# Performance work log

Hardware: AMD Instinct MI355X
Metric: run time of the kernel (lower is better)

The kernel has to match this reference:

```python
import jax, jax.numpy as jnp
import numpy as np

B, T, C, H = 32, 2048, 1024, 64


def setup_inputs() -> dict:
    key = jax.random.key(0)
    k1, k2, k3, k4 = jax.random.split(key, 4)
    x = jax.random.normal(k1, (B, T, C), dtype=jnp.float32)
    # nn.Linear(C, H, bias=False) weights, stored here as [C, H] for x @ W
    s = 1.0 / np.sqrt(C)
    Wk = jax.random.uniform(k2, (C, H), jnp.float32, -s, s)
    Wq = jax.random.uniform(k3, (C, H), jnp.float32, -s, s)
    Wv = jax.random.uniform(k4, (C, H), jnp.float32, -s, s)
    return {"x": x, "Wk": Wk, "Wq": Wq, "Wv": Wv}


def reference(x, Wk, Wq, Wv):
    # projections: [B,T,C] @ [C,H] -> [B,T,H]
    k = jnp.einsum('btc,ch->bth', x, Wk)
    q = jnp.einsum('btc,ch->bth', x, Wq)
    v = jnp.einsum('btc,ch->bth', x, Wv)
    Hd = k.shape[-1]
    # attention scores [B,T,T], scaled by head_size^-0.5
    scores = jnp.einsum('bqh,bkh->bqk', q, k) * (Hd ** -0.5)
    # causal mask: masked_fill where triu(ones, 1)==1 -> -inf (mask strict upper triangle)
    Tq = x.shape[1]
    causal = jnp.tril(jnp.ones((Tq, Tq), dtype=bool))  # True = keep
    scores = jnp.where(causal, scores, -jnp.inf)
    attn = jax.nn.softmax(scores, axis=-1)
    # dropout: identity in eval/reference mode
    out = jnp.einsum('bqk,bkh->bqh', attn, v)
    return out
```

## Files before the change

kernel.cpp:

```cpp
#include <hip/hip_runtime.h>

typedef short bf16x8 __attribute__((ext_vector_type(8)));
typedef float f32x4 __attribute__((ext_vector_type(4)));

#define B_ 32
#define T_ 2048
#define C_ 1024
#define H_ 64

__device__ __forceinline__ ushort f2bf(float f) {
  union { float f; unsigned u; } v; v.f = f;
  unsigned u = v.u;
  return (ushort)((u + 0x7FFFu + ((u >> 16) & 1u)) >> 16);
}

__device__ __forceinline__ void async_copy16(void* lds, const void* g) {
  __builtin_amdgcn_global_load_lds(
      (const __attribute__((address_space(1))) unsigned int*)g,
      (__attribute__((address_space(3))) unsigned int*)lds, 16, 0, 0);
}

__global__ __launch_bounds__(256) void wconv_kernel(
    const float* __restrict__ Wk, const float* __restrict__ Wq,
    const float* __restrict__ Wv, ushort* __restrict__ Wt) {
  int idx = blockIdx.x * 256 + threadIdx.x;
  if (idx >= 3 * 64 * C_) return;
  int n = idx >> 10, c = idx & 1023;
  int mat = n >> 6, h = n & 63;
  const float* W = (mat == 0) ? Wk : (mat == 1 ? Wq : Wv);
  float v = W[c * 64 + h];
  if (mat == 1) v *= 0.18033688011112042f;
  Wt[idx] = f2bf(v);
}

__global__ __launch_bounds__(256) void qkv_kernel(
    const float* __restrict__ x, const ushort* __restrict__ Wt,
    ushort* __restrict__ Kb, ushort* __restrict__ Qb, ushort* __restrict__ Vt) {
  __shared__ __align__(16) float As[128 * 64];
  __shared__ __align__(16) ushort Bs[192 * 64];
  int tid = threadIdx.x;
  int wave = tid >> 6, lane = tid & 63, quad = lane >> 4, l16 = lane & 15;
  int r0 = blockIdx.x * 128;

  f32x4 acc[2][12];
#pragma unroll
  for (int rt = 0; rt < 2; ++rt)
#pragma unroll
    for (int nt = 0; nt < 12; ++nt) acc[rt][nt] = (f32x4){0.f, 0.f, 0.f, 0.f};

  for (int k0 = 0; k0 < C_; k0 += 64) {
    __syncthreads();
#pragma unroll
    for (int i = 0; i < 8; ++i) {
      int id = tid + 256 * i;
      int arow = id >> 4, acp = id & 15;
      int ac = acp ^ (arow & 15);
      async_copy16((char*)As + id * 16,
                   x + (size_t)(r0 + arow) * C_ + k0 + ac * 4);
    }
#pragma unroll
    for (int i = 0; i < 6; ++i) {
      int id = tid + 256 * i;
      int bn = id >> 3, bcp = id & 7;
      int bc = bcp ^ (bn & 7);
      async_copy16((char*)Bs + id * 16,
                   Wt + (size_t)bn * C_ + k0 + bc * 8);
    }
    __syncthreads();

#pragma unroll
    for (int ks = 0; ks < 2; ++ks) {
      bf16x8 af[2];
#pragma unroll
      for (int rt = 0; rt < 2; ++rt) {
        int row = wave * 32 + rt * 16 + l16;
        int c0 = ks * 8 + quad * 2;
        f32x4 a0 = *(const f32x4*)(As + row * 64 + ((c0 ^ l16) << 2));
        f32x4 a1 = *(const f32x4*)(As + row * 64 + (((c0 + 1) ^ l16) << 2));
        bf16x8 t;
        t[0] = (short)f2bf(a0[0]); t[1] = (short)f2bf(a0[1]);
        t[2] = (short)f2bf(a0[2]); t[3] = (short)f2bf(a0[3]);
        t[4] = (short)f2bf(a1[0]); t[5] = (short)f2bf(a1[1]);
        t[6] = (short)f2bf(a1[2]); t[7] = (short)f2bf(a1[3]);
        af[rt] = t;
      }
#pragma unroll
      for (int nt = 0; nt < 12; ++nt) {
        int n = nt * 16 + l16;
        int cb = ks * 4 + quad;
        bf16x8 bf = *(const bf16x8*)(Bs + n * 64 + ((cb ^ (l16 & 7)) << 3));
        acc[0][nt] = __builtin_amdgcn_mfma_f32_16x16x32_bf16(af[0], bf, acc[0][nt], 0, 0, 0);
        acc[1][nt] = __builtin_amdgcn_mfma_f32_16x16x32_bf16(af[1], bf, acc[1][nt], 0, 0, 0);
      }
    }
  }

  int b = r0 >> 11;
#pragma unroll
  for (int rt = 0; rt < 2; ++rt) {
    int rowbase = r0 + wave * 32 + rt * 16 + quad * 4;
#pragma unroll
    for (int nt = 0; nt < 12; ++nt) {
      int mat = nt >> 2;
      int h = (nt & 3) * 16 + l16;
#pragma unroll
      for (int r = 0; r < 4; ++r) {
        ushort val = f2bf(acc[rt][nt][r]);
        int row = rowbase + r;
        if (mat == 0)      Kb[(size_t)row * H_ + h] = val;
        else if (mat == 1) Qb[(size_t)row * H_ + h] = val;
        else               Vt[(size_t)b * H_ * T_ + (size_t)h * T_ + (row & (T_ - 1))] = val;
      }
    }
  }
}

__global__ __launch_bounds__(256) void attn_kernel(
    const ushort* __restrict__ Qb, const ushort* __restrict__ Kb,
    const ushort* __restrict__ Vt, float* __restrict__ out) {
  __shared__ __align__(16) ushort Pl[4 * 32 * 80];

  int tid = threadIdx.x;
  int wave = tid >> 6, lane = tid & 63, quad = lane >> 4, l16 = lane & 15;
  int batch = blockIdx.y;
  int q0 = blockIdx.x * 128 + wave * 32;
  const ushort* Qbase = Qb + (size_t)batch * T_ * H_;
  const ushort* Kbase = Kb + (size_t)batch * T_ * H_;
  const ushort* Vbase = Vt + (size_t)batch * H_ * T_;
  ushort* Pw = Pl + wave * 32 * 80;

  bf16x8 qf[2][2];
#pragma unroll
  for (int rt = 0; rt < 2; ++rt) {
    const ushort* qr = Qbase + (size_t)(q0 + rt * 16 + l16) * H_;
    qf[rt][0] = *(const bf16x8*)(qr + quad * 8);
    qf[rt][1] = *(const bf16x8*)(qr + 32 + quad * 8);
  }

  f32x4 o[2][4];
  float m_i[2][4], l_i[2][4];
#pragma unroll
  for (int rt = 0; rt < 2; ++rt)
#pragma unroll
    for (int i = 0; i < 4; ++i) {
      o[rt][i] = (f32x4){0.f, 0.f, 0.f, 0.f};
      m_i[rt][i] = -1e30f; l_i[rt][i] = 0.f;
    }

  int jb_last = (q0 + 31) >> 6;
  for (int jb = 0; jb <= jb_last; ++jb) {
    int j0 = jb * 64;

    f32x4 sv[2][4];
#pragma unroll
    for (int nt = 0; nt < 4; ++nt) {
      const ushort* kr = Kbase + (size_t)(j0 + nt * 16 + l16) * H_;
      bf16x8 kf0 = *(const bf16x8*)(kr + quad * 8);
      bf16x8 kf1 = *(const bf16x8*)(kr + 32 + quad * 8);
#pragma unroll
      for (int rt = 0; rt < 2; ++rt) {
        f32x4 z = (f32x4){0.f, 0.f, 0.f, 0.f};
        z = __builtin_amdgcn_mfma_f32_16x16x32_bf16(qf[rt][0], kf0, z, 0, 0, 0);
        z = __builtin_amdgcn_mfma_f32_16x16x32_bf16(qf[rt][1], kf1, z, 0, 0, 0);
        sv[rt][nt] = z;
      }
    }

    if (jb == jb_last) {
#pragma unroll
      for (int rt = 0; rt < 2; ++rt) {
        int rowg = q0 + rt * 16 + quad * 4;
#pragma unroll
        for (int nt = 0; nt < 4; ++nt) {
          int col = j0 + nt * 16 + l16;
#pragma unroll
          for (int rr = 0; rr < 4; ++rr)
            if (col > rowg + rr) sv[rt][nt][rr] = -1e30f;
        }
      }
    }

    float alpha[2][4];
#pragma unroll
    for (int rt = 0; rt < 2; ++rt)
#pragma unroll
      for (int rr = 0; rr < 4; ++rr) {
        float v = fmaxf(fmaxf(sv[rt][0][rr], sv[rt][1][rr]),
                        fmaxf(sv[rt][2][rr], sv[rt][3][rr]));
        v = fmaxf(v, __shfl_xor(v, 1));
        v = fmaxf(v, __shfl_xor(v, 2));
        v = fmaxf(v, __shfl_xor(v, 4));
        v = fmaxf(v, __shfl_xor(v, 8));
        float mn = fmaxf(m_i[rt][rr], v);
        alpha[rt][rr] = exp2f(m_i[rt][rr] - mn);
        m_i[rt][rr] = mn;
      }

#pragma unroll
    for (int rt = 0; rt < 2; ++rt) {
      float rsum[4] = {0.f, 0.f, 0.f, 0.f};
#pragma unroll
      for (int nt = 0; nt < 4; ++nt)
#pragma unroll
        for (int rr = 0; rr < 4; ++rr) {
          float p = exp2f(sv[rt][nt][rr] - m_i[rt][rr]);
          rsum[rr] += p;
          Pw[(rt * 16 + quad * 4 + rr) * 80 + nt * 16 + l16] = f2bf(p);
        }
#pragma unroll
      for (int rr = 0; rr < 4; ++rr)
        l_i[rt][rr] = alpha[rt][rr] * l_i[rt][rr] + rsum[rr];
#pragma unroll
      for (int ht = 0; ht < 4; ++ht)
#pragma unroll
        for (int rr = 0; rr < 4; ++rr) o[rt][ht][rr] *= alpha[rt][rr];
    }

    bf16x8 pf[2][2];
#pragma unroll
    for (int rt = 0; rt < 2; ++rt) {
      pf[rt][0] = *(const bf16x8*)(&Pw[(rt * 16 + l16) * 80 + quad * 8]);
      pf[rt][1] = *(const bf16x8*)(&Pw[(rt * 16 + l16) * 80 + 32 + quad * 8]);
    }
#pragma unroll
    for (int ht = 0; ht < 4; ++ht) {
      const ushort* vr = Vbase + (size_t)(ht * 16 + l16) * T_ + j0;
      bf16x8 vf0 = *(const bf16x8*)(vr + quad * 8);
      bf16x8 vf1 = *(const bf16x8*)(vr + 32 + quad * 8);
#pragma unroll
      for (int rt = 0; rt < 2; ++rt) {
        o[rt][ht] = __builtin_amdgcn_mfma_f32_16x16x32_bf16(pf[rt][0], vf0, o[rt][ht], 0, 0, 0);
        o[rt][ht] = __builtin_amdgcn_mfma_f32_16x16x32_bf16(pf[rt][1], vf1, o[rt][ht], 0, 0, 0);
      }
    }
  }

#pragma unroll
  for (int rt = 0; rt < 2; ++rt)
#pragma unroll
    for (int rr = 0; rr < 4; ++rr) {
      float v = l_i[rt][rr];
      v += __shfl_xor(v, 1);
      v += __shfl_xor(v, 2);
      v += __shfl_xor(v, 4);
      v += __shfl_xor(v, 8);
      l_i[rt][rr] = v;
    }
#pragma unroll
  for (int rt = 0; rt < 2; ++rt) {
    int rowbase = q0 + rt * 16 + quad * 4;
#pragma unroll
    for (int ht = 0; ht < 4; ++ht)
#pragma unroll
      for (int rr = 0; rr < 4; ++rr)
        out[((size_t)batch * T_ + rowbase + rr) * H_ + ht * 16 + l16] =
            o[rt][ht][rr] / l_i[rt][rr];
  }
}

extern "C" void kernel_launch(void* const* d_in, const int* in_sizes, int n_in,
                              void* d_out, int out_size, void* d_ws, size_t ws_size,
                              hipStream_t stream) {
  const float* x  = (const float*)d_in[0];
  const float* Wk = (const float*)d_in[1];
  const float* Wq = (const float*)d_in[2];
  const float* Wv = (const float*)d_in[3];
  float* out = (float*)d_out;

  ushort* Wt = (ushort*)d_ws;
  ushort* Kb = (ushort*)((char*)d_ws + (1 << 19));
  ushort* Qb = Kb + (size_t)B_ * T_ * H_;
  ushort* Vt = Qb + (size_t)B_ * T_ * H_;

  hipLaunchKernelGGL(wconv_kernel, dim3(768), dim3(256), 0, stream, Wk, Wq, Wv, Wt);
  hipLaunchKernelGGL(qkv_kernel, dim3(512), dim3(256), 0, stream, x, Wt, Kb, Qb, Vt);
  hipLaunchKernelGGL(attn_kernel, dim3(16, 32), dim3(256), 0, stream, Qb, Kb, Vt, out);
}
```

Measured before the change: 514.6 us.

## Restructure QKV projection staging and shrink attention tiles to one 16-row strip per wave

Result: slower. 667.3 us (+29.7%).

```diff
diff --git a/kernel.cpp b/kernel.cpp
--- a/kernel.cpp
+++ b/kernel.cpp
@@ -36,8 +36,7 @@
 __global__ __launch_bounds__(256) void qkv_kernel(
     const float* __restrict__ x, const ushort* __restrict__ Wt,
     ushort* __restrict__ Kb, ushort* __restrict__ Qb, ushort* __restrict__ Vt) {
-  __shared__ __align__(16) float As[128 * 64];
-  __shared__ __align__(16) ushort Bs[192 * 64];
+  __shared__ __align__(16) float As[2][128 * 64];
   int tid = threadIdx.x;
   int wave = tid >> 6, lane = tid & 63, quad = lane >> 4, l16 = lane & 15;
   int r0 = blockIdx.x * 128;
@@ -48,49 +47,52 @@
 #pragma unroll
     for (int nt = 0; nt < 12; ++nt) acc[rt][nt] = (f32x4){0.f, 0.f, 0.f, 0.f};
 
-  for (int k0 = 0; k0 < C_; k0 += 64) {
+  for (int k0 = 0; k0 < C_; k0 += 128) {
     __syncthreads();
 #pragma unroll
     for (int i = 0; i < 8; ++i) {
       int id = tid + 256 * i;
-      int arow = id >> 4, acp = id & 15;
-      int ac = acp ^ (arow & 15);
-      async_copy16((char*)As + id * 16,
-                   x + (size_t)(r0 + arow) * C_ + k0 + ac * 4);
-    }
-#pragma unroll
-    for (int i = 0; i < 6; ++i) {
+      int r = id >> 4, p = id & 15;
+      int c = p ^ (r & 15);
+      async_copy16((char*)(&As[0][0]) + id * 16,
+                   x + (size_t)(r0 + r) * C_ + k0 + c * 4);
+    }
+#pragma unroll
+    for (int i = 0; i < 8; ++i) {
       int id = tid + 256 * i;
-      int bn = id >> 3, bcp = id & 7;
-      int bc = bcp ^ (bn & 7);
-      async_copy16((char*)Bs + id * 16,
-                   Wt + (size_t)bn * C_ + k0 + bc * 8);
+      int r = id >> 4, p = id & 15;
+      int c = p ^ (r & 15);
+      async_copy16((char*)(&As[1][0]) + id * 16,
+                   x + (size_t)(r0 + r) * C_ + k0 + 64 + c * 4);
     }
     __syncthreads();
 
 #pragma unroll
-    for (int ks = 0; ks < 2; ++ks) {
-      bf16x8 af[2];
-#pragma unroll
-      for (int rt = 0; rt < 2; ++rt) {
-        int row = wave * 32 + rt * 16 + l16;
-        int c0 = ks * 8 + quad * 2;
-        f32x4 a0 = *(const f32x4*)(As + row * 64 + ((c0 ^ l16) << 2));
-        f32x4 a1 = *(const f32x4*)(As + row * 64 + (((c0 + 1) ^ l16) << 2));
-        bf16x8 t;
-        t[0] = (short)f2bf(a0[0]); t[1] = (short)f2bf(a0[1]);
-        t[2] = (short)f2bf(a0[2]); t[3] = (short)f2bf(a0[3]);
-        t[4] = (short)f2bf(a1[0]); t[5] = (short)f2bf(a1[1]);
-        t[6] = (short)f2bf(a1[2]); t[7] = (short)f2bf(a1[3]);
-        af[rt] = t;
-      }
-#pragma unroll
-      for (int nt = 0; nt < 12; ++nt) {
-        int n = nt * 16 + l16;
-        int cb = ks * 4 + quad;
-        bf16x8 bf = *(const bf16x8*)(Bs + n * 64 + ((cb ^ (l16 & 7)) << 3));
-        acc[0][nt] = __builtin_amdgcn_mfma_f32_16x16x32_bf16(af[0], bf, acc[0][nt], 0, 0, 0);
-        acc[1][nt] = __builtin_amdgcn_mfma_f32_16x16x32_bf16(af[1], bf, acc[1][nt], 0, 0, 0);
+    for (int half = 0; half < 2; ++half) {
+      int kbase = k0 + half * 64;
+#pragma unroll
+      for (int ks = 0; ks < 2; ++ks) {
+        bf16x8 af[2];
+#pragma unroll
+        for (int rt = 0; rt < 2; ++rt) {
+          int row = wave * 32 + rt * 16 + l16;
+          int c0 = ks * 8 + quad * 2;
+          f32x4 a0 = *(const f32x4*)(&As[half][row * 64 + ((c0 ^ l16) << 2)]);
+          f32x4 a1 = *(const f32x4*)(&As[half][row * 64 + (((c0 + 1) ^ l16) << 2)]);
+          bf16x8 t;
+          t[0] = (short)f2bf(a0[0]); t[1] = (short)f2bf(a0[1]);
+          t[2] = (short)f2bf(a0[2]); t[3] = (short)f2bf(a0[3]);
+          t[4] = (short)f2bf(a1[0]); t[5] = (short)f2bf(a1[1]);
+          t[6] = (short)f2bf(a1[2]); t[7] = (short)f2bf(a1[3]);
+          af[rt] = t;
+        }
+#pragma unroll
+        for (int nt = 0; nt < 12; ++nt) {
+          bf16x8 bf = *(const bf16x8*)(Wt + (size_t)(nt * 16 + l16) * C_ +
+                                       kbase + ks * 32 + quad * 8);
+          acc[0][nt] = __builtin_amdgcn_mfma_f32_16x16x32_bf16(af[0], bf, acc[0][nt], 0, 0, 0);
+          acc[1][nt] = __builtin_amdgcn_mfma_f32_16x16x32_bf16(af[1], bf, acc[1][nt], 0, 0, 0);
+        }
       }
     }
   }
@@ -103,13 +105,16 @@
     for (int nt = 0; nt < 12; ++nt) {
       int mat = nt >> 2;
       int h = (nt & 3) * 16 + l16;
-#pragma unroll
-      for (int r = 0; r < 4; ++r) {
-        ushort val = f2bf(acc[rt][nt][r]);
-        int row = rowbase + r;
-        if (mat == 0)      Kb[(size_t)row * H_ + h] = val;
-        else if (mat == 1) Qb[(size_t)row * H_ + h] = val;
-        else               Vt[(size_t)b * H_ * T_ + (size_t)h * T_ + (row & (T_ - 1))] = val;
+      if (mat == 2) {
+        ushort4 pv;
+        pv.x = f2bf(acc[rt][nt][0]); pv.y = f2bf(acc[rt][nt][1]);
+        pv.z = f2bf(acc[rt][nt][2]); pv.w = f2bf(acc[rt][nt][3]);
+        *(ushort4*)(&Vt[(size_t)b * H_ * T_ + (size_t)h * T_ + (rowbase & (T_ - 1))]) = pv;
+      } else {
+        ushort* dst = (mat == 0) ? Kb : Qb;
+#pragma unroll
+        for (int r = 0; r < 4; ++r)
+          dst[(size_t)(rowbase + r) * H_ + h] = f2bf(acc[rt][nt][r]);
       }
     }
   }
@@ -118,144 +123,119 @@
 __global__ __launch_bounds__(256) void attn_kernel(
     const ushort* __restrict__ Qb, const ushort* __restrict__ Kb,
     const ushort* __restrict__ Vt, float* __restrict__ out) {
-  __shared__ __align__(16) ushort Pl[4 * 32 * 80];
+  __shared__ __align__(16) ushort Pl[4 * 16 * 80];
 
   int tid = threadIdx.x;
   int wave = tid >> 6, lane = tid & 63, quad = lane >> 4, l16 = lane & 15;
-  int batch = blockIdx.y;
-  int q0 = blockIdx.x * 128 + wave * 32;
+  int bx = blockIdx.x, by = blockIdx.y;
+  int batch = (bx & 7) + 8 * (by & 3);
+  int qseg = (bx >> 3) + 4 * (by >> 2);
+  int q0 = qseg * 64 + wave * 16;
   const ushort* Qbase = Qb + (size_t)batch * T_ * H_;
   const ushort* Kbase = Kb + (size_t)batch * T_ * H_;
   const ushort* Vbase = Vt + (size_t)batch * H_ * T_;
-  ushort* Pw = Pl + wave * 32 * 80;
-
-  bf16x8 qf[2][2];
-#pragma unroll
-  for (int rt = 0; rt < 2; ++rt) {
-    const ushort* qr = Qbase + (size_t)(q0 + rt * 16 + l16) * H_;
-    qf[rt][0] = *(const bf16x8*)(qr + quad * 8);
-    qf[rt][1] = *(const bf16x8*)(qr + 32 + quad * 8);
-  }
-
-  f32x4 o[2][4];
-  float m_i[2][4], l_i[2][4];
-#pragma unroll
-  for (int rt = 0; rt < 2; ++rt)
-#pragma unroll
-    for (int i = 0; i < 4; ++i) {
-      o[rt][i] = (f32x4){0.f, 0.f, 0.f, 0.f};
-      m_i[rt][i] = -1e30f; l_i[rt][i] = 0.f;
-    }
-
-  int jb_last = (q0 + 31) >> 6;
+  ushort* Pw = Pl + wave * 16 * 80;
+
+  const ushort* qr = Qbase + (size_t)(q0 + l16) * H_;
+  bf16x8 qf0 = *(const bf16x8*)(qr + quad * 8);
+  bf16x8 qf1 = *(const bf16x8*)(qr + 32 + quad * 8);
+
+  f32x4 o[4];
+  float m_i[4], l_i[4];
+#pragma unroll
+  for (int i = 0; i < 4; ++i) {
+    o[i] = (f32x4){0.f, 0.f, 0.f, 0.f};
+    m_i[i] = -1e30f; l_i[i] = 0.f;
+  }
+
+  int jb_last = q0 >> 6;
   for (int jb = 0; jb <= jb_last; ++jb) {
     int j0 = jb * 64;
 
-    f32x4 sv[2][4];
+    bf16x8 vf[4][2];
+#pragma unroll
+    for (int ht = 0; ht < 4; ++ht) {
+      const ushort* vr = Vbase + (size_t)(ht * 16 + l16) * T_ + j0;
+      vf[ht][0] = *(const bf16x8*)(vr + quad * 8);
+      vf[ht][1] = *(const bf16x8*)(vr + 32 + quad * 8);
+    }
+
+    f32x4 sv[4];
 #pragma unroll
     for (int nt = 0; nt < 4; ++nt) {
       const ushort* kr = Kbase + (size_t)(j0 + nt * 16 + l16) * H_;
       bf16x8 kf0 = *(const bf16x8*)(kr + quad * 8);
       bf16x8 kf1 = *(const bf16x8*)(kr + 32 + quad * 8);
-#pragma unroll
-      for (int rt = 0; rt < 2; ++rt) {
-        f32x4 z = (f32x4){0.f, 0.f, 0.f, 0.f};
-        z = __builtin_amdgcn_mfma_f32_16x16x32_bf16(qf[rt][0], kf0, z, 0, 0, 0);
-        z = __builtin_amdgcn_mfma_f32_16x16x32_bf16(qf[rt][1], kf1, z, 0, 0, 0);
-        sv[rt][nt] = z;
-      }
+      f32x4 z = (f32x4){0.f, 0.f, 0.f, 0.f};
+      z = __builtin_amdgcn_mfma_f32_16x16x32_bf16(qf0, kf0, z, 0, 0, 0);
+      z = __builtin_amdgcn_mfma_f32_16x16x32_bf16(qf1, kf1, z, 0, 0, 0);
+      sv[nt] = z;
     }
 
     if (jb == jb_last) {
-#pragma unroll
-      for (int rt = 0; rt < 2; ++rt) {
-        int rowg = q0 + rt * 16 + quad * 4;
-#pragma unroll
-        for (int nt = 0; nt < 4; ++nt) {
-          int col = j0 + nt * 16 + l16;
-#pragma unroll
-          for (int rr = 0; rr < 4; ++rr)
-            if (col > rowg + rr) sv[rt][nt][rr] = -1e30f;
-        }
-      }
-    }
-
-    float alpha[2][4];
-#pragma unroll
-    for (int rt = 0; rt < 2; ++rt)
+      int rowg = q0 + quad * 4;
+#pragma unroll
+      for (int nt = 0; nt < 4; ++nt) {
+        int col = j0 + nt * 16 + l16;
+#pragma unroll
+        for (int rr = 0; rr < 4; ++rr)
+          if (col > rowg + rr) sv[nt][rr] = -1e30f;
+      }
+    }
+
+    float alpha[4];
+#pragma unroll
+    for (int rr = 0; rr < 4; ++rr) {
+      float v = fmaxf(fmaxf(sv[0][rr], sv[1][rr]), fmaxf(sv[2][rr], sv[3][rr]));
+      v = fmaxf(v, __shfl_xor(v, 1));
+      v = fmaxf(v, __shfl_xor(v, 2));
+      v = fmaxf(v, __shfl_xor(v, 4));
+      v = fmaxf(v, __shfl_xor(v, 8));
+      float mn = fmaxf(m_i[rr], v);
+      alpha[rr] = exp2f(m_i[rr] - mn);
+      m_i[rr] = mn;
+    }
+    float rsum[4] = {0.f, 0.f, 0.f, 0.f};
+#pragma unroll
+    for (int nt = 0; nt < 4; ++nt)
 #pragma unroll
       for (int rr = 0; rr < 4; ++rr) {
-        float v = fmaxf(fmaxf(sv[rt][0][rr], sv[rt][1][rr]),
-                        fmaxf(sv[rt][2][rr], sv[rt][3][rr]));
-        v = fmaxf(v, __shfl_xor(v, 1));
-        v = fmaxf(v, __shfl_xor(v, 2));
-        v = fmaxf(v, __shfl_xor(v, 4));
-        v = fmaxf(v, __shfl_xor(v, 8));
-        float mn = fmaxf(m_i[rt][rr], v);
-        alpha[rt][rr] = exp2f(m_i[rt][rr] - mn);
-        m_i[rt][rr] = mn;
-      }
-
-#pragma unroll
-    for (int rt = 0; rt < 2; ++rt) {
-      float rsum[4] = {0.f, 0.f, 0.f, 0.f};
-#pragma unroll
-      for (int nt = 0; nt < 4; ++nt)
-#pragma unroll
-        for (int rr = 0; rr < 4; ++rr) {
-          float p = exp2f(sv[rt][nt][rr] - m_i[rt][rr]);
-          rsum[rr] += p;
-          Pw[(rt * 16 + quad * 4 + rr) * 80 + nt * 16 + l16] = f2bf(p);
-        }
-#pragma unroll
-      for (int rr = 0; rr < 4; ++rr)
-        l_i[rt][rr] = alpha[rt][rr] * l_i[rt][rr] + rsum[rr];
-#pragma unroll
-      for (int ht = 0; ht < 4; ++ht)
-#pragma unroll
-        for (int rr = 0; rr < 4; ++rr) o[rt][ht][rr] *= alpha[rt][rr];
-    }
-
-    bf16x8 pf[2][2];
-#pragma unroll
-    for (int rt = 0; rt < 2; ++rt) {
-      pf[rt][0] = *(const bf16x8*)(&Pw[(rt * 16 + l16) * 80 + quad * 8]);
-      pf[rt][1] = *(const bf16x8*)(&Pw[(rt * 16 + l16) * 80 + 32 + quad * 8]);
-    }
+        float p = exp2f(sv[nt][rr] - m_i[rr]);
+        rsum[rr] += p;
+        Pw[(quad * 4 + rr) * 80 + nt * 16 + l16] = f2bf(p);
+      }
+#pragma unroll
+    for (int rr = 0; rr < 4; ++rr) l_i[rr] = alpha[rr] * l_i[rr] + rsum[rr];
+#pragma unroll
+    for (int ht = 0; ht < 4; ++ht)
+#pragma unroll
+      for (int rr = 0; rr < 4; ++rr) o[ht][rr] *= alpha[rr];
+
+    bf16x8 pf0 = *(const bf16x8*)(&Pw[l16 * 80 + quad * 8]);
+    bf16x8 pf1 = *(const bf16x8*)(&Pw[l16 * 80 + 32 + quad * 8]);
 #pragma unroll
     for (int ht = 0; ht < 4; ++ht) {
-      const ushort* vr = Vbase + (size_t)(ht * 16 + l16) * T_ + j0;
-      bf16x8 vf0 = *(const bf16x8*)(vr + quad * 8);
-      bf16x8 vf1 = *(const bf16x8*)(vr + 32 + quad * 8);
-#pragma unroll
-      for (int rt = 0; rt < 2; ++rt) {
-        o[rt][ht] = __builtin_amdgcn_mfma_f32_16x16x32_bf16(pf[rt][0], vf0, o[rt][ht], 0, 0, 0);
-        o[rt][ht] = __builtin_amdgcn_mfma_f32_16x16x32_bf16(pf[rt][1], vf1, o[rt][ht], 0, 0, 0);
-      }
-    }
-  }
-
-#pragma unroll
-  for (int rt = 0; rt < 2; ++rt)
-#pragma unroll
-    for (int rr = 0; rr < 4; ++rr) {
-      float v = l_i[rt][rr];
-      v += __shfl_xor(v, 1);
-      v += __shfl_xor(v, 2);
-      v += __shfl_xor(v, 4);
-      v += __shfl_xor(v, 8);
-      l_i[rt][rr] = v;
-    }
-#pragma unroll
-  for (int rt = 0; rt < 2; ++rt) {
-    int rowbase = q0 + rt * 16 + quad * 4;
-#pragma unroll
-    for (int ht = 0; ht < 4; ++ht)
-#pragma unroll
-      for (int rr = 0; rr < 4; ++rr)
-        out[((size_t)batch * T_ + rowbase + rr) * H_ + ht * 16 + l16] =
-            o[rt][ht][rr] / l_i[rt][rr];
-  }
+      o[ht] = __builtin_amdgcn_mfma_f32_16x16x32_bf16(pf0, vf[ht][0], o[ht], 0, 0, 0);
+      o[ht] = __builtin_amdgcn_mfma_f32_16x16x32_bf16(pf1, vf[ht][1], o[ht], 0, 0, 0);
+    }
+  }
+
+#pragma unroll
+  for (int rr = 0; rr < 4; ++rr) {
+    float v = l_i[rr];
+    v += __shfl_xor(v, 1);
+    v += __shfl_xor(v, 2);
+    v += __shfl_xor(v, 4);
+    v += __shfl_xor(v, 8);
+    l_i[rr] = __builtin_amdgcn_rcpf(v);
+  }
+  int rowbase = q0 + quad * 4;
+#pragma unroll
+  for (int ht = 0; ht < 4; ++ht)
+#pragma unroll
+    for (int rr = 0; rr < 4; ++rr)
+      out[((size_t)batch * T_ + rowbase + rr) * H_ + ht * 16 + l16] =
+          o[ht][rr] * l_i[rr];
 }
 
 extern "C" void kernel_launch(void* const* d_in, const int* in_sizes, int n_in,
@@ -274,5 +254,5 @@
 
   hipLaunchKernelGGL(wconv_kernel, dim3(768), dim3(256), 0, stream, Wk, Wq, Wv, Wt);
   hipLaunchKernelGGL(qkv_kernel, dim3(512), dim3(256), 0, stream, x, Wt, Kb, Qb, Vt);
-  hipLaunchKernelGGL(attn_kernel, dim3(16, 32), dim3(256), 0, stream, Qb, Kb, Vt, out);
-}
+  hipLaunchKernelGGL(attn_kernel, dim3(32, 32), dim3(256), 0, stream, Qb, Kb, Vt, out);
+}
```
